# Kernel optimization log

Measured on AMD Instinct MI355X. Metric: run time of the kernel, lower is better.

Reference implementation:

```python
import jax, jax.numpy as jnp
import numpy as np

B, T, C = 4, 1024, 512
H, HD = 8, 64
NE, K = 8, 2
FF = 4 * C


def setup_inputs() -> dict:
    key = jax.random.key(0)
    ks = jax.random.split(key, 16)
    s = 0.02
    return {
        "x": jax.random.normal(ks[0], (B, T, C), jnp.float32),
        "ln1_g": jnp.ones((C,), jnp.float32),
        "ln1_b": jnp.zeros((C,), jnp.float32),
        "ln2_g": jnp.ones((C,), jnp.float32),
        "ln2_b": jnp.zeros((C,), jnp.float32),
        "Wq": jax.random.normal(ks[1], (H, C, HD), jnp.float32) * s,
        "Wk": jax.random.normal(ks[2], (H, C, HD), jnp.float32) * s,
        "Wv": jax.random.normal(ks[3], (H, C, HD), jnp.float32) * s,
        "Wp": jax.random.normal(ks[4], (H * HD, C), jnp.float32) * s,
        "bp": jnp.zeros((C,), jnp.float32),
        "Wr": jax.random.normal(ks[5], (C, NE), jnp.float32) * s,
        "br": jnp.zeros((NE,), jnp.float32),
        "W1": jax.random.normal(ks[6], (NE, C, FF), jnp.float32) * s,
        "b1": jnp.zeros((NE, FF), jnp.float32),
        "W2": jax.random.normal(ks[7], (NE, FF, C), jnp.float32) * s,
        "b2": jnp.zeros((NE, C), jnp.float32),
    }


def _ln(x, g, b, eps=1e-5):
    mu = jnp.mean(x, axis=-1, keepdims=True)
    var = jnp.var(x, axis=-1, keepdims=True)
    return (x - mu) * jax.lax.rsqrt(var + eps) * g + b


def reference(x, ln1_g, ln1_b, ln2_g, ln2_b, Wq, Wk, Wv, Wp, bp, Wr, br, W1, b1, W2, b2):
    # --- multi-head causal attention (all heads stacked) ---
    h = _ln(x, ln1_g, ln1_b)
    q = jnp.einsum("btc,hcd->bhtd", h, Wq)
    k = jnp.einsum("btc,hcd->bhtd", h, Wk)
    v = jnp.einsum("btc,hcd->bhtd", h, Wv)
    wei = jnp.einsum("bhtd,bhsd->bhts", q, k) / np.sqrt(HD).astype(np.float32)
    causal = jnp.tril(jnp.ones((T, T), bool))
    wei = jnp.where(causal, wei, -jnp.inf)
    wei = jax.nn.softmax(wei, axis=-1)
    attn = jnp.einsum("bhts,bhsd->bhtd", wei, v)  # [B,H,T,HD]
    attn = attn.transpose(0, 2, 1, 3).reshape(B, T, H * HD)
    x2 = x + attn @ Wp + bp

    # --- SparseMoE: dense all-experts compute, masked top-k combine ---
    h2 = _ln(x2, ln2_g, ln2_b)
    scores = h2 @ Wr + br  # [B,T,NE]
    topk_scores, indices = jax.lax.top_k(scores, K)
    # scatter top-k scores into zeros (rest stays 0), then softmax over experts
    mask = jnp.sum(jax.nn.one_hot(indices, NE, dtype=scores.dtype) * topk_scores[..., None], axis=-2)
    router = jax.nn.softmax(mask, axis=-1)  # [B,T,NE]
    hid = jax.nn.relu(jnp.einsum("btc,ecf->btef", h2, W1) + b1)  # [B,T,NE,FF]
    eo = jnp.einsum("btef,efc->btec", hid, W2) + b2  # [B,T,NE,C]
    moe = jnp.einsum("bte,btec->btc", router, eo)
    return x2 + moe
```

## Files before the change

kernel.cpp:

```cpp
#include <hip/hip_runtime.h>


typedef unsigned short u16;
typedef __attribute__((ext_vector_type(8))) short s16x8;
typedef __attribute__((ext_vector_type(4))) float f32x4;

__device__ __forceinline__ u16 f2bf(float f) {
  union { float f; unsigned u; } v; v.f = f;
  unsigned r = v.u + 0x7fffu + ((v.u >> 16) & 1u);
  return (u16)(r >> 16);
}
__device__ __forceinline__ float bf2f(u16 h) {
  union { unsigned u; float f; } v; v.u = ((unsigned)h) << 16;
  return v.f;
}

#define GLDS16(g, s) __builtin_amdgcn_global_load_lds( \
    (const __attribute__((address_space(1))) void*)(g), \
    (__attribute__((address_space(3))) void*)(s), 16, 0, 0)

#define MFMA16(a, b, c) __builtin_amdgcn_mfma_f32_16x16x32_bf16((a), (b), (c), 0, 0, 0)

__global__ __launch_bounds__(256) void transpose_k(
    const float* __restrict__ in, u16* __restrict__ out,
    int R, int C, long long ibs, long long obs, float scale)
{
  __shared__ float tile[32][33];
  in  += (long long)blockIdx.z * ibs;
  out += (long long)blockIdx.z * obs;
  const int c0 = blockIdx.x * 32, r0 = blockIdx.y * 32;
  const int tx = threadIdx.x, ty = threadIdx.y;
  #pragma unroll
  for (int i = 0; i < 4; ++i)
    tile[ty + i*8][tx] = in[(size_t)(r0 + ty + i*8) * C + c0 + tx];
  __syncthreads();
  #pragma unroll
  for (int i = 0; i < 4; ++i)
    out[(size_t)(c0 + ty + i*8) * R + r0 + tx] = f2bf(tile[tx][ty + i*8] * scale);
}

__global__ __launch_bounds__(256) void vtrans_k(
    const u16* __restrict__ qkv, u16* __restrict__ vt)
{
  __shared__ u16 tile[32][33];
  const int bh = blockIdx.z, b = bh >> 3, h = bh & 7;
  const int t0 = blockIdx.x * 32, d0 = blockIdx.y * 32;
  const int tx = threadIdx.x, ty = threadIdx.y;
  #pragma unroll
  for (int i = 0; i < 4; ++i)
    tile[ty + i*8][tx] = qkv[(size_t)(b*1024 + t0 + ty + i*8) * 1536 + 1024 + h*64 + d0 + tx];
  __syncthreads();
  #pragma unroll
  for (int i = 0; i < 4; ++i)
    vt[(size_t)bh*65536 + (size_t)(d0 + ty + i*8) * 1024 + t0 + tx] = tile[tx][ty + i*8];
}

__global__ __launch_bounds__(256) void ln_k(
    const float* __restrict__ x, const float* __restrict__ g,
    const float* __restrict__ b, u16* __restrict__ o)
{
  const int row = blockIdx.x, t = threadIdx.x;
  const float* xr = x + (size_t)row * 512;
  const float a0 = xr[t], a1 = xr[t + 256];
  float s = a0 + a1, ss = a0*a0 + a1*a1;
  #pragma unroll
  for (int off = 1; off < 64; off <<= 1) {
    s  += __shfl_xor(s, off);
    ss += __shfl_xor(ss, off);
  }
  __shared__ float rs[4], rq[4];
  const int w = t >> 6;
  if ((t & 63) == 0) { rs[w] = s; rq[w] = ss; }
  __syncthreads();
  s  = rs[0] + rs[1] + rs[2] + rs[3];
  ss = rq[0] + rq[1] + rq[2] + rq[3];
  const float mu = s * (1.f/512.f);
  const float var = ss * (1.f/512.f) - mu*mu;
  const float rstd = rsqrtf(var + 1e-5f);
  o[(size_t)row*512 + t]       = f2bf((a0 - mu) * rstd * g[t]     + b[t]);
  o[(size_t)row*512 + t + 256] = f2bf((a1 - mu) * rstd * g[t+256] + b[t+256]);
}

template<int EPI>
__global__ __launch_bounds__(256) void gemm64(
    const u16* __restrict__ A, const u16* __restrict__ Bt,
    int M, int N, int K, int lda, int ldb,
    u16* __restrict__ obf, float* __restrict__ oa,
    const float* __restrict__ bias, const float* __restrict__ extra, int e0)
{
  __shared__ u16 Asm[128*64];
  __shared__ u16 Bsm[128*64];
  const int t = threadIdx.x;
  const int l = t & 63;
  const int wid = t >> 6, wr = wid >> 1, wc = wid & 1;
  const int lrow = l & 15, lhi = l >> 4;
  const int m0 = blockIdx.x * 128, n0 = blockIdx.y * 128;

  const f32x4 z4 = {0.f, 0.f, 0.f, 0.f};
  f32x4 acc[4][4];
  #pragma unroll
  for (int i = 0; i < 4; ++i)
    #pragma unroll
    for (int j = 0; j < 4; ++j) acc[i][j] = z4;

  const u16* ga = A  + (size_t)(m0 + (t >> 3)) * lda + (t & 7) * 8;
  const u16* gb = Bt + (size_t)(n0 + (t >> 3)) * ldb + (t & 7) * 8;

  for (int k0 = 0; k0 < K; k0 += 64) {
    #pragma unroll
    for (int i = 0; i < 4; ++i) {
      GLDS16(ga + (size_t)i*32*lda + k0, (char*)Asm + i*4096 + t*16);
      GLDS16(gb + (size_t)i*32*ldb + k0, (char*)Bsm + i*4096 + t*16);
    }
    __syncthreads();
    #pragma unroll
    for (int kh = 0; kh < 2; ++kh) {
      s16x8 af[4], bfr[4];
      #pragma unroll
      for (int i = 0; i < 4; ++i)
        af[i]  = *(const s16x8*)(Asm + (wr*64 + i*16 + lrow)*64 + kh*32 + lhi*8);
      #pragma unroll
      for (int j = 0; j < 4; ++j)
        bfr[j] = *(const s16x8*)(Bsm + (wc*64 + j*16 + lrow)*64 + kh*32 + lhi*8);
      #pragma unroll
      for (int i = 0; i < 4; ++i)
        #pragma unroll
        for (int j = 0; j < 4; ++j)
          acc[i][j] = MFMA16(af[i], bfr[j], acc[i][j]);
    }
    __syncthreads();
  }

  #pragma unroll
  for (int i = 0; i < 4; ++i) {
    const int rbase = m0 + wr*64 + i*16 + lhi*4;
    #pragma unroll
    for (int j = 0; j < 4; ++j) {
      const int col = n0 + wc*64 + j*16 + lrow;
      #pragma unroll
      for (int rr = 0; rr < 4; ++rr) {
        const int row = rbase + rr;
        const float v = acc[i][j][rr];
        if (EPI == 0) {
          obf[(size_t)row*N + col] = f2bf(v);
        } else if (EPI == 1) {
          const float r = extra[(size_t)row*8 + e0 + (col >> 11)];
          obf[(size_t)row*N + col] = f2bf(fmaxf(v + bias[col], 0.f) * r);
        } else {
          oa[(size_t)row*N + col] = v + bias[col] + extra[(size_t)row*N + col];
        }
      }
    }
  }
}

template<int NKT, int EPI>
__global__ __launch_bounds__(512, 2) void gemm8p(
    const u16* __restrict__ A, const u16* __restrict__ Bt,
    int lda, int ldb,
    u16* __restrict__ obf,
    const float* __restrict__ bias, const float* __restrict__ rout)
{
  __shared__ u16 Lds[2][2][256*64];
  const int t = threadIdx.x, l = t & 63;
  const int wid = t >> 6, wm = wid >> 2, wn = wid & 3;
  const int lrow = l & 15, lhi = l >> 4;

  int m0, n0, zz = 0;
  {
    const int bid = blockIdx.x;
    const int r = bid & 7, k = bid >> 3;
    if (EPI == 1) { m0 = (k >> 3) * 256; n0 = (r * 8 + (k & 7)) * 256; }
    else { zz = r + (k >> 3) * 8; m0 = ((k & 7) >> 1) * 256; n0 = (k & 1) * 256; }
  }
  const u16* Ab = A  + (size_t)m0 * lda + (EPI == 4 ? zz * 512 : 0);
  const u16* Bb = Bt + (size_t)n0 * ldb + (EPI == 4 ? zz * 512 : 0);

  const int tr = t >> 3;
  const int sc = ((t & 7) ^ (tr & 7)) * 8;

#define STG(bf, kt, hx) do { \
    const int X_ = (hx) >> 1, h_ = (hx) & 1; \
    const u16* s_ = X_ ? Bb : Ab; \
    const int ld_ = X_ ? ldb : lda; \
    char* d_ = (char*)&Lds[bf][X_][0] + h_*16384 + t*16; \
    GLDS16(s_ + (size_t)(h_*128 + tr) * ld_ + (kt)*64 + sc, d_); \
    GLDS16(s_ + (size_t)(h_*128 + 64 + tr) * ld_ + (kt)*64 + sc, d_ + 8192); \
  } while (0)

#define RD(Ls, row, kb) (*(const s16x8*)((const char*)(Ls) + (row)*128 + ((kb) ^ (((row)&7)<<4))))

  f32x4 acc[8][4];
  const f32x4 z4 = {0.f, 0.f, 0.f, 0.f};
  #pragma unroll
  for (int i = 0; i < 8; ++i)
    #pragma unroll
    for (int j = 0; j < 4; ++j) acc[i][j] = z4;

  #pragma unroll
  for (int kt = 0; kt < 2; ++kt)
    #pragma unroll
    for (int hx = 0; hx < 4; ++hx) STG(kt & 1, kt, hx);
  asm volatile("s_waitcnt vmcnt(8)" ::: "memory");
  __builtin_amdgcn_sched_barrier(0);
  __builtin_amdgcn_s_barrier();

  s16x8 frA[2][4], frB[2][2];
  #pragma unroll
  for (int X = 0; X < NKT; ++X) {
    const u16* As = &Lds[X & 1][0][0];
    const u16* Bs = &Lds[X & 1][1][0];
    #pragma unroll
    for (int q = 0; q < 4; ++q) {
      const int mh = q >> 1, nh = q & 1;
      if (nh == 0) {
        #pragma unroll
        for (int kk = 0; kk < 2; ++kk)
          #pragma unroll
          for (int mf = 0; mf < 4; ++mf) {
            const int row = wm*128 + (mh*4 + mf)*16 + lrow;
            frA[kk][mf] = RD(As, row, kk*64 + lhi*16);
          }
      }
      #pragma unroll
      for (int kk = 0; kk < 2; ++kk)
        #pragma unroll
        for (int nf = 0; nf < 2; ++nf) {
          const int row = wn*64 + (nh*2 + nf)*16 + lrow;
          frB[kk][nf] = RD(Bs, row, kk*64 + lhi*16);
        }
      {
        const int P = 4*X + q;
        if (P >= 3) {
          const int kts = ((P - 3) >> 2) + 2, hh = (P - 3) & 3;
          if (kts < NKT) STG(kts & 1, kts, hh);
        }
      }
      __builtin_amdgcn_s_barrier();
      asm volatile("s_waitcnt lgkmcnt(0)" ::: "memory");
      __builtin_amdgcn_sched_barrier(0);
      __builtin_amdgcn_s_setprio(1);
      #pragma unroll
      for (int kk = 0; kk < 2; ++kk)
        #pragma unroll
        for (int mf = 0; mf < 4; ++mf)
          #pragma unroll
          for (int nf = 0; nf < 2; ++nf)
            acc[mh*4 + mf][nh*2 + nf] =
                MFMA16(frA[kk][mf], frB[kk][nf], acc[mh*4 + mf][nh*2 + nf]);
      __builtin_amdgcn_s_setprio(0);
      if (q == 3 && X + 1 < NKT) {
        if (X + 2 < NKT) asm volatile("s_waitcnt vmcnt(2)" ::: "memory");
        else             asm volatile("s_waitcnt vmcnt(0)" ::: "memory");
        __builtin_amdgcn_sched_barrier(0);
      }
      __builtin_amdgcn_s_barrier();
    }
  }
#undef STG
#undef RD

  u16* outp = (EPI == 4) ? obf + (size_t)zz * 1024 * 512 : obf;
  #pragma unroll
  for (int mf = 0; mf < 8; ++mf) {
    const int rbase = m0 + wm*128 + mf*16 + lhi*4;
    #pragma unroll
    for (int nf = 0; nf < 4; ++nf) {
      const int col = n0 + wn*64 + nf*16 + lrow;
      #pragma unroll
      for (int rr = 0; rr < 4; ++rr) {
        const int row = rbase + rr;
        const float v = acc[mf][nf][rr];
        if (EPI == 1) {
          const float r = rout[(size_t)row*8 + (col >> 11)];
          outp[(size_t)row*16384 + col] = f2bf(fmaxf(v + bias[col], 0.f) * r);
        } else {
          outp[(size_t)row*512 + col] = f2bf(v);
        }
      }
    }
  }
}

__global__ __launch_bounds__(256) void combineQ_k(
    float* __restrict__ outq, const u16* __restrict__ P,
    const float* __restrict__ routq, const float* __restrict__ b2)
{
  const int row = blockIdx.x, t = threadIdx.x;
  float r[8];
  #pragma unroll
  for (int e = 0; e < 8; ++e) r[e] = routq[(size_t)row*8 + e];
  #pragma unroll
  for (int cc = 0; cc < 2; ++cc) {
    const int c = t + cc*256;
    float v = outq[(size_t)row*512 + c];
    #pragma unroll
    for (int z = 0; z < 32; ++z) v += bf2f(P[(size_t)z*524288 + (size_t)row*512 + c]);
    #pragma unroll
    for (int e = 0; e < 8; ++e) v += r[e] * b2[(size_t)e*512 + c];
    outq[(size_t)row*512 + c] = v;
  }
}

__global__ __launch_bounds__(256) void gemm2_k(
    const u16* __restrict__ hid, const u16* __restrict__ w2t,
    u16* __restrict__ P, int e0, int accum)
{
  __shared__ u16 Asm[128*64];
  __shared__ u16 Bsm[64*64];
  const int t = threadIdx.x;
  const int l = t & 63;
  const int wid = t >> 6, wr = wid >> 1, wc = wid & 1;
  const int lrow = l & 15, lhi = l >> 4;
  const int m0 = blockIdx.x * 128, n0 = blockIdx.y * 64, z = blockIdx.z;

  const u16* A  = hid + z * 2048;
  const u16* Bt = w2t + (size_t)(e0 + z) * 512 * 2048;
  u16* Pz = P + (size_t)z * 4096 * 512;

  const f32x4 z4 = {0.f, 0.f, 0.f, 0.f};
  f32x4 acc[4][2];
  #pragma unroll
  for (int i = 0; i < 4; ++i) { acc[i][0] = z4; acc[i][1] = z4; }

  const u16* ga = A  + (size_t)(m0 + (t >> 3)) * 4096 + (t & 7) * 8;
  const u16* gb = Bt + (size_t)(n0 + (t >> 3)) * 2048 + (t & 7) * 8;

  for (int k0 = 0; k0 < 2048; k0 += 64) {
    #pragma unroll
    for (int i = 0; i < 4; ++i)
      GLDS16(ga + (size_t)i*32*4096 + k0, (char*)Asm + i*4096 + t*16);
    #pragma unroll
    for (int i = 0; i < 2; ++i)
      GLDS16(gb + (size_t)i*32*2048 + k0, (char*)Bsm + i*4096 + t*16);
    __syncthreads();
    #pragma unroll
    for (int kh = 0; kh < 2; ++kh) {
      s16x8 af[4], bfr[2];
      #pragma unroll
      for (int i = 0; i < 4; ++i)
        af[i]  = *(const s16x8*)(Asm + (wr*64 + i*16 + lrow)*64 + kh*32 + lhi*8);
      #pragma unroll
      for (int j = 0; j < 2; ++j)
        bfr[j] = *(const s16x8*)(Bsm + (wc*32 + j*16 + lrow)*64 + kh*32 + lhi*8);
      #pragma unroll
      for (int i = 0; i < 4; ++i)
        #pragma unroll
        for (int j = 0; j < 2; ++j)
          acc[i][j] = MFMA16(af[i], bfr[j], acc[i][j]);
    }
    __syncthreads();
  }

  #pragma unroll
  for (int i = 0; i < 4; ++i) {
    const int rbase = m0 + wr*64 + i*16 + lhi*4;
    #pragma unroll
    for (int j = 0; j < 2; ++j) {
      const int col = n0 + wc*32 + j*16 + lrow;
      #pragma unroll
      for (int rr = 0; rr < 4; ++rr) {
        const size_t idx = (size_t)(rbase + rr) * 512 + col;
        const float old = accum ? bf2f(Pz[idx]) : 0.f;
        Pz[idx] = f2bf(old + acc[i][j][rr]);
      }
    }
  }
}

__global__ __launch_bounds__(256) void combineB_k(
    float* __restrict__ out, const u16* __restrict__ P,
    const float* __restrict__ rout, const float* __restrict__ b2)
{
  const int row = blockIdx.x, t = threadIdx.x;
  float r[8];
  #pragma unroll
  for (int e = 0; e < 8; ++e) r[e] = rout[(size_t)row*8 + e];
  #pragma unroll
  for (int cc = 0; cc < 2; ++cc) {
    const int c = t + cc*256;
    const size_t idx = (size_t)row*512 + c;
    float v = out[idx] + bf2f(P[idx]) + bf2f(P[(size_t)4096*512 + idx]);
    #pragma unroll
    for (int e = 0; e < 8; ++e) v += r[e] * b2[(size_t)e*512 + c];
    out[idx] = v;
  }
}

__global__ __launch_bounds__(256) void attn_k(
    const u16* __restrict__ qkv, const u16* __restrict__ vt, u16* __restrict__ o)
{
  const int bid = blockIdx.x;
  const int xcd = bid & 7, rr_ = bid >> 3;
  const int bh = (rr_ >> 4) * 8 + xcd;
  const int qb = rr_ & 15;
  const int b = bh >> 3, h = bh & 7;
  const int t = threadIdx.x, l = t & 63, w = t >> 6;
  const int lrow = l & 15, lhi = l >> 4;
  const int t0w = qb*64 + w*16;

  __shared__ u16 Ksm[2][64*64];
  __shared__ u16 Vsm[2][64*64];
  __shared__ u16 Psm[4][16][72];

  const u16* qrow = qkv + (size_t)(b*1024 + t0w + lrow) * 1536 + h*64 + lhi*8;
  s16x8 qf0 = *(const s16x8*)qrow;
  s16x8 qf1 = *(const s16x8*)(qrow + 32);

  const f32x4 z4 = {0.f,0.f,0.f,0.f};
  float m[4], sl[4];
  f32x4 oacc[4];
  #pragma unroll
  for (int i = 0; i < 4; ++i) { m[i] = -1e30f; sl[i] = 0.f; oacc[i] = z4; }

  const int trow = t >> 3;
  const int csw = ((t & 7) ^ (trow & 7)) * 8;
  const u16* gk = qkv + (size_t)(b*1024 + trow) * 1536 + 512 + h*64 + csw;
  const u16* gv = vt + (size_t)bh*65536 + (size_t)trow*1024 + csw;
  const int nt = qb + 1;

#define ASTAGE(buf, s0) do { \
    _Pragma("unroll") \
    for (int i = 0; i < 2; ++i) { \
      GLDS16(gk + (size_t)((s0) + i*32) * 1536, (char*)Ksm[buf] + i*4096 + t*16); \
      GLDS16(gv + (s0) + (size_t)(i*32)*1024,   (char*)Vsm[buf] + i*4096 + t*16); \
    } } while (0)

  ASTAGE(0, 0);
  for (int kv = 0; kv < nt; ++kv) {
    const int s0 = kv * 64;
    if (kv + 1 < nt) {
      ASTAGE((kv + 1) & 1, s0 + 64);
      asm volatile("s_waitcnt vmcnt(4)" ::: "memory");
    } else {
      asm volatile("s_waitcnt vmcnt(0)" ::: "memory");
    }
    __builtin_amdgcn_s_barrier();
    __builtin_amdgcn_sched_barrier(0);
    const u16* Ks = Ksm[kv & 1];
    const u16* Vs = Vsm[kv & 1];

    f32x4 sacc[4] = {z4, z4, z4, z4};
    #pragma unroll
    for (int n = 0; n < 4; ++n) {
      const int r = n*16 + lrow;
      s16x8 kf0 = *(const s16x8*)((const char*)Ks + r*128 + ((lhi*16) ^ ((r & 7) << 4)));
      s16x8 kf1 = *(const s16x8*)((const char*)Ks + r*128 + ((64 + lhi*16) ^ ((r & 7) << 4)));
      sacc[n] = MFMA16(qf0, kf0, sacc[n]);
      sacc[n] = MFMA16(qf1, kf1, sacc[n]);
    }
    if (s0 + 63 > t0w) {
      #pragma unroll
      for (int n = 0; n < 4; ++n)
        #pragma unroll
        for (int rr = 0; rr < 4; ++rr)
          if (s0 + n*16 + lrow > t0w + lhi*4 + rr) sacc[n][rr] = -1e30f;
    }
    float pm[4];
    #pragma unroll
    for (int rr = 0; rr < 4; ++rr)
      pm[rr] = fmaxf(fmaxf(sacc[0][rr], sacc[1][rr]), fmaxf(sacc[2][rr], sacc[3][rr]));
    #pragma unroll
    for (int rr = 0; rr < 4; ++rr) {
      pm[rr] = fmaxf(pm[rr], __shfl_xor(pm[rr], 1));
      pm[rr] = fmaxf(pm[rr], __shfl_xor(pm[rr], 2));
      pm[rr] = fmaxf(pm[rr], __shfl_xor(pm[rr], 4));
      pm[rr] = fmaxf(pm[rr], __shfl_xor(pm[rr], 8));
    }
    float p[4][4], ps[4], scv[4];
    #pragma unroll
    for (int rr = 0; rr < 4; ++rr) {
      const float mn = fmaxf(m[rr], pm[rr]);
      scv[rr] = __expf(m[rr] - mn);
      m[rr] = mn;
      ps[rr] = 0.f;
      #pragma unroll
      for (int n = 0; n < 4; ++n) {
        p[n][rr] = __expf(sacc[n][rr] - mn);
        ps[rr] += p[n][rr];
      }
    }
    #pragma unroll
    for (int rr = 0; rr < 4; ++rr) {
      ps[rr] += __shfl_xor(ps[rr], 1);
      ps[rr] += __shfl_xor(ps[rr], 2);
      ps[rr] += __shfl_xor(ps[rr], 4);
      ps[rr] += __shfl_xor(ps[rr], 8);
      sl[rr] = sl[rr] * scv[rr] + ps[rr];
    }
    #pragma unroll
    for (int ct = 0; ct < 4; ++ct) {
      f32x4 t4 = oacc[ct];
      #pragma unroll
      for (int rr = 0; rr < 4; ++rr) t4[rr] *= scv[rr];
      oacc[ct] = t4;
    }
    #pragma unroll
    for (int n = 0; n < 4; ++n)
      #pragma unroll
      for (int rr = 0; rr < 4; ++rr)
        Psm[w][lhi*4 + rr][n*16 + lrow] = f2bf(p[n][rr]);
    asm volatile("s_waitcnt lgkmcnt(0)" ::: "memory");
    __builtin_amdgcn_sched_barrier(0);
    s16x8 pa0 = *(const s16x8*)&Psm[w][lrow][lhi*8];
    s16x8 pa1 = *(const s16x8*)&Psm[w][lrow][32 + lhi*8];
    #pragma unroll
    for (int ct = 0; ct < 4; ++ct) {
      const int r = ct*16 + lrow;
      s16x8 vb0 = *(const s16x8*)((const char*)Vs + r*128 + ((lhi*16) ^ ((r & 7) << 4)));
      s16x8 vb1 = *(const s16x8*)((const char*)Vs + r*128 + ((64 + lhi*16) ^ ((r & 7) << 4)));
      oacc[ct] = MFMA16(pa0, vb0, oacc[ct]);
      oacc[ct] = MFMA16(pa1, vb1, oacc[ct]);
    }
    __builtin_amdgcn_s_barrier();
    __builtin_amdgcn_sched_barrier(0);
  }
#undef ASTAGE
  #pragma unroll
  for (int ct = 0; ct < 4; ++ct)
    #pragma unroll
    for (int rr = 0; rr < 4; ++rr) {
      const int row = b*1024 + t0w + lhi*4 + rr;
      o[(size_t)row*512 + h*64 + ct*16 + lrow] = f2bf(oacc[ct][rr] / sl[rr]);
    }
}

__global__ __launch_bounds__(256) void router_k(
    const float* __restrict__ x2, const float* __restrict__ g,
    const float* __restrict__ b, const float* __restrict__ Wr,
    const float* __restrict__ br, float* __restrict__ rt)
{
  const int l = threadIdx.x & 63, w = threadIdx.x >> 6;
  const int tkn = blockIdx.x * 4 + w;
  const float* xr = x2 + (size_t)tkn * 512;
  float v[8];
  float s = 0.f, ss = 0.f;
  #pragma unroll
  for (int i = 0; i < 8; ++i) {
    v[i] = xr[l*8 + i];
    s += v[i]; ss += v[i]*v[i];
  }
  #pragma unroll
  for (int off = 1; off < 64; off <<= 1) {
    s  += __shfl_xor(s, off);
    ss += __shfl_xor(ss, off);
  }
  const float mu = s * (1.f/512.f);
  const float var = ss * (1.f/512.f) - mu*mu;
  const float rstd = rsqrtf(var + 1e-5f);
  float acc[8];
  #pragma unroll
  for (int e = 0; e < 8; ++e) acc[e] = 0.f;
  #pragma unroll
  for (int i = 0; i < 8; ++i) {
    const int c = l*8 + i;
    const float hv = (v[i] - mu) * rstd * g[c] + b[c];
    const float* wrow = Wr + (size_t)c * 8;
    #pragma unroll
    for (int e = 0; e < 8; ++e) acc[e] += hv * wrow[e];
  }
  #pragma unroll
  for (int e = 0; e < 8; ++e) {
    #pragma unroll
    for (int off = 1; off < 64; off <<= 1) acc[e] += __shfl_xor(acc[e], off);
    acc[e] += br[e];
  }
  int e1 = 0;
  #pragma unroll
  for (int e = 1; e < 8; ++e) if (acc[e] > acc[e1]) e1 = e;
  int e2 = (e1 == 0) ? 1 : 0;
  #pragma unroll
  for (int e = 0; e < 8; ++e) if (e != e1 && acc[e] > acc[e2]) e2 = e;
  const float mx = fmaxf(acc[e1], 0.f);
  float Z = 0.f;
  #pragma unroll
  for (int e = 0; e < 8; ++e) {
    const float mv = (e == e1 || e == e2) ? acc[e] : 0.f;
    Z += __expf(mv - mx);
  }
  if (l < 8) {
    const float mv = (l == e1 || l == e2) ? acc[l] : 0.f;
    rt[(size_t)tkn * 8 + l] = __expf(mv - mx) / Z;
  }
}

extern "C" void kernel_launch(void* const* d_in, const int* in_sizes, int n_in,
                              void* d_out, int out_size, void* d_ws, size_t ws_size,
                              hipStream_t stream) {
  const float* x    = (const float*)d_in[0];
  const float* ln1g = (const float*)d_in[1];
  const float* ln1b = (const float*)d_in[2];
  const float* ln2g = (const float*)d_in[3];
  const float* ln2b = (const float*)d_in[4];
  const float* Wq   = (const float*)d_in[5];
  const float* Wk   = (const float*)d_in[6];
  const float* Wv   = (const float*)d_in[7];
  const float* Wp   = (const float*)d_in[8];
  const float* bp   = (const float*)d_in[9];
  const float* Wr   = (const float*)d_in[10];
  const float* br   = (const float*)d_in[11];
  const float* W1   = (const float*)d_in[12];
  const float* b1   = (const float*)d_in[13];
  const float* W2   = (const float*)d_in[14];
  const float* b2   = (const float*)d_in[15];
  float* out = (float*)d_out;

  const int pathN = (ws_size >= (size_t)104988672) ? 1 : 0;

  char* ws = (char*)d_ws;
  size_t off = 0;
  auto alloc = [&](size_t bytes) -> char* {
    char* p = ws + off;
    off += (bytes + 255) & ~(size_t)255;
    return p;
  };
  u16* w1_t = (u16*)alloc((size_t)8*2048*512*2);
  u16* w2f  = (u16*)alloc((size_t)8*512*2048*2);
  u16* h2b  = (u16*)alloc((size_t)4096*512*2);
  float* rout = (float*)alloc((size_t)4096*8*4);
  u16* hidq = (u16*)alloc((size_t)4096*4096*2);
  u16* Ppl  = (u16*)alloc((size_t)2*4096*512*2);
  u16* wqkv_t = (u16*)hidq;
  u16* wp_t   = (u16*)((char*)hidq + 1572864);
  u16* hb     = (u16*)((char*)hidq + 2097152);
  u16* attnb  = (u16*)((char*)hidq + 6291456);
  u16* qkvb   = (u16*)((char*)hidq + 10485760);
  u16* vtb    = (u16*)((char*)hidq + 23068672);

  const dim3 tb(32, 8);
  transpose_k<<<dim3(2,16,8),  tb, 0, stream>>>(Wq, wqkv_t,              512,   64, 512*64,  (long long)64*512, 0.125f);
  transpose_k<<<dim3(2,16,8),  tb, 0, stream>>>(Wk, wqkv_t + 512*512,    512,   64, 512*64,  (long long)64*512, 1.f);
  transpose_k<<<dim3(2,16,8),  tb, 0, stream>>>(Wv, wqkv_t + 2*512*512,  512,   64, 512*64,  (long long)64*512, 1.f);
  transpose_k<<<dim3(16,16,1), tb, 0, stream>>>(Wp, wp_t,                512,  512, 0, 0, 1.f);
  transpose_k<<<dim3(64,16,8), tb, 0, stream>>>(W1, w1_t,                512, 2048, (long long)512*2048, (long long)2048*512, 1.f);
  if (pathN)
    transpose_k<<<dim3(16,512,1), tb, 0, stream>>>(W2, w2f, 16384, 512, 0, 0, 1.f);
  else
    transpose_k<<<dim3(16,64,8), tb, 0, stream>>>(W2, w2f, 2048, 512, (long long)2048*512, (long long)512*2048, 1.f);

  ln_k<<<4096, 256, 0, stream>>>(x, ln1g, ln1b, hb);
  gemm64<0><<<dim3(32,12), 256, 0, stream>>>(hb, wqkv_t, 4096, 1536, 512, 512, 512,
                                             qkvb, nullptr, nullptr, nullptr, 0);
  vtrans_k<<<dim3(32,2,32), tb, 0, stream>>>(qkvb, vtb);
  attn_k<<<512, 256, 0, stream>>>(qkvb, vtb, attnb);
  gemm64<2><<<dim3(32,4), 256, 0, stream>>>(attnb, wp_t, 4096, 512, 512, 512, 512,
                                            nullptr, out, bp, x, 0);
  ln_k<<<4096, 256, 0, stream>>>(out, ln2g, ln2b, h2b);
  router_k<<<1024, 256, 0, stream>>>(out, ln2g, ln2b, Wr, br, rout);

  if (pathN) {
    for (int q = 0; q < 4; ++q) {
      gemm8p<8,1><<<256, 512, 0, stream>>>(h2b + (size_t)q*1024*512, w1_t, 512, 512,
                                           hidq, b1, rout + (size_t)q*8192);
      gemm8p<8,4><<<256, 512, 0, stream>>>(hidq, w2f, 16384, 16384,
                                           Ppl, nullptr, nullptr);
      combineQ_k<<<1024, 256, 0, stream>>>(out + (size_t)q*1024*512, Ppl,
                                           rout + (size_t)q*8192, b2);
    }
  } else {
    for (int p = 0; p < 4; ++p) {
      const int e0 = 2*p;
      gemm64<1><<<dim3(32,32), 256, 0, stream>>>(h2b, w1_t + (size_t)e0*2048*512,
                                                 4096, 4096, 512, 512, 512,
                                                 hidq, nullptr, b1 + (size_t)e0*2048, rout, e0);
      gemm2_k<<<dim3(32,8,2), 256, 0, stream>>>(hidq, w2f, Ppl, e0, p > 0 ? 1 : 0);
    }
    combineB_k<<<4096, 256, 0, stream>>>(out, Ppl, rout, b2);
  }
}
```

Measured before the change: 327.5 us.

## Double-buffer GEMM loads, fuse QKV transposes and LN2 into router, vectorize combine

Replaces the single-buffered gemm64 with gemm2p, which double-buffers LDS tiles and waits on vmcnt so global loads of the next tile overlap MFMA work. The output projection now uses a 64-wide N tile, giving twice as many blocks. The three QKV weight transposes are merged into one launch, and the router kernel now also writes the bf16 LN2 output, which removes the separate ln_k pass. combineQ_k reads packed bf16 pairs, and Ppl is sized to 32 partials on pathN. The cost is doubled LDS per block, which may reduce occupancy.

Measured after the change: 314.7 us. -3.9%, faster.

```diff
diff --git a/kernel.cpp b/kernel.cpp
--- a/kernel.cpp
+++ b/kernel.cpp
@@ -37,6 +37,26 @@
   #pragma unroll
   for (int i = 0; i < 4; ++i)
     out[(size_t)(c0 + ty + i*8) * R + r0 + tx] = f2bf(tile[tx][ty + i*8] * scale);
+}
+
+__global__ __launch_bounds__(256) void transqkv_k(
+    const float* __restrict__ Wq, const float* __restrict__ Wk,
+    const float* __restrict__ Wv, u16* __restrict__ out)
+{
+  __shared__ float tile[32][33];
+  const int z = blockIdx.z, which = z >> 3, head = z & 7;
+  const float* in = (which == 0 ? Wq : (which == 1 ? Wk : Wv)) + (size_t)head * 512 * 64;
+  u16* o = out + (size_t)which * 512 * 512 + (size_t)head * 64 * 512;
+  const float scale = (which == 0) ? 0.125f : 1.f;
+  const int c0 = blockIdx.x * 32, r0 = blockIdx.y * 32;
+  const int tx = threadIdx.x, ty = threadIdx.y;
+  #pragma unroll
+  for (int i = 0; i < 4; ++i)
+    tile[ty + i*8][tx] = in[(size_t)(r0 + ty + i*8) * 64 + c0 + tx];
+  __syncthreads();
+  #pragma unroll
+  for (int i = 0; i < 4; ++i)
+    o[(size_t)(c0 + ty + i*8) * 512 + r0 + tx] = f2bf(tile[tx][ty + i*8] * scale);
 }
 
 __global__ __launch_bounds__(256) void vtrans_k(
@@ -81,62 +101,81 @@
   o[(size_t)row*512 + t + 256] = f2bf((a1 - mu) * rstd * g[t+256] + b[t+256]);
 }
 
-template<int EPI>
-__global__ __launch_bounds__(256) void gemm64(
+template<int BN, int EPI>
+__global__ __launch_bounds__(256) void gemm2p(
     const u16* __restrict__ A, const u16* __restrict__ Bt,
     int M, int N, int K, int lda, int ldb,
     u16* __restrict__ obf, float* __restrict__ oa,
     const float* __restrict__ bias, const float* __restrict__ extra, int e0)
 {
-  __shared__ u16 Asm[128*64];
-  __shared__ u16 Bsm[128*64];
-  const int t = threadIdx.x;
-  const int l = t & 63;
+  constexpr int NB = BN / 32;
+  constexpr int SB = BN / 32;
+  __shared__ u16 Asm[2][128*64];
+  __shared__ u16 Bsm[2][BN*64];
+  const int t = threadIdx.x, l = t & 63;
   const int wid = t >> 6, wr = wid >> 1, wc = wid & 1;
   const int lrow = l & 15, lhi = l >> 4;
-  const int m0 = blockIdx.x * 128, n0 = blockIdx.y * 128;
+  const int m0 = blockIdx.x * 128, n0 = blockIdx.y * BN;
 
   const f32x4 z4 = {0.f, 0.f, 0.f, 0.f};
-  f32x4 acc[4][4];
+  f32x4 acc[4][NB];
   #pragma unroll
   for (int i = 0; i < 4; ++i)
     #pragma unroll
-    for (int j = 0; j < 4; ++j) acc[i][j] = z4;
+    for (int j = 0; j < NB; ++j) acc[i][j] = z4;
 
   const u16* ga = A  + (size_t)(m0 + (t >> 3)) * lda + (t & 7) * 8;
   const u16* gb = Bt + (size_t)(n0 + (t >> 3)) * ldb + (t & 7) * 8;
 
-  for (int k0 = 0; k0 < K; k0 += 64) {
-    #pragma unroll
-    for (int i = 0; i < 4; ++i) {
-      GLDS16(ga + (size_t)i*32*lda + k0, (char*)Asm + i*4096 + t*16);
-      GLDS16(gb + (size_t)i*32*ldb + k0, (char*)Bsm + i*4096 + t*16);
-    }
-    __syncthreads();
+#define STG2(buf, k0) do { \
+    _Pragma("unroll") \
+    for (int i = 0; i < 4; ++i) \
+      GLDS16(ga + (size_t)(i*32)*lda + (k0), (char*)Asm[buf] + i*4096 + t*16); \
+    _Pragma("unroll") \
+    for (int i = 0; i < SB; ++i) \
+      GLDS16(gb + (size_t)(i*32)*ldb + (k0), (char*)Bsm[buf] + i*4096 + t*16); \
+  } while (0)
+
+  const int NT = K >> 6;
+  STG2(0, 0);
+  for (int tt = 0; tt < NT; ++tt) {
+    if (tt + 1 < NT) {
+      STG2((tt + 1) & 1, (tt + 1) * 64);
+      if constexpr (BN == 128) asm volatile("s_waitcnt vmcnt(8)" ::: "memory");
+      else                     asm volatile("s_waitcnt vmcnt(6)" ::: "memory");
+    } else {
+      asm volatile("s_waitcnt vmcnt(0)" ::: "memory");
+    }
+    __builtin_amdgcn_sched_barrier(0);
+    __builtin_amdgcn_s_barrier();
+    const u16* As = Asm[tt & 1];
+    const u16* Bs = Bsm[tt & 1];
     #pragma unroll
     for (int kh = 0; kh < 2; ++kh) {
-      s16x8 af[4], bfr[4];
+      s16x8 af[4], bfr[NB];
       #pragma unroll
       for (int i = 0; i < 4; ++i)
-        af[i]  = *(const s16x8*)(Asm + (wr*64 + i*16 + lrow)*64 + kh*32 + lhi*8);
-      #pragma unroll
-      for (int j = 0; j < 4; ++j)
-        bfr[j] = *(const s16x8*)(Bsm + (wc*64 + j*16 + lrow)*64 + kh*32 + lhi*8);
+        af[i]  = *(const s16x8*)(As + (wr*64 + i*16 + lrow)*64 + kh*32 + lhi*8);
+      #pragma unroll
+      for (int j = 0; j < NB; ++j)
+        bfr[j] = *(const s16x8*)(Bs + (wc*(BN/2) + j*16 + lrow)*64 + kh*32 + lhi*8);
       #pragma unroll
       for (int i = 0; i < 4; ++i)
         #pragma unroll
-        for (int j = 0; j < 4; ++j)
+        for (int j = 0; j < NB; ++j)
           acc[i][j] = MFMA16(af[i], bfr[j], acc[i][j]);
     }
-    __syncthreads();
-  }
+    __builtin_amdgcn_s_barrier();
+    __builtin_amdgcn_sched_barrier(0);
+  }
+#undef STG2
 
   #pragma unroll
   for (int i = 0; i < 4; ++i) {
     const int rbase = m0 + wr*64 + i*16 + lhi*4;
     #pragma unroll
-    for (int j = 0; j < 4; ++j) {
-      const int col = n0 + wc*64 + j*16 + lrow;
+    for (int j = 0; j < NB; ++j) {
+      const int col = n0 + wc*(BN/2) + j*16 + lrow;
       #pragma unroll
       for (int rr = 0; rr < 4; ++rr) {
         const int row = rbase + rr;
@@ -287,19 +326,25 @@
     const float* __restrict__ routq, const float* __restrict__ b2)
 {
   const int row = blockIdx.x, t = threadIdx.x;
+  const int c = t * 2;
   float r[8];
   #pragma unroll
   for (int e = 0; e < 8; ++e) r[e] = routq[(size_t)row*8 + e];
-  #pragma unroll
-  for (int cc = 0; cc < 2; ++cc) {
-    const int c = t + cc*256;
-    float v = outq[(size_t)row*512 + c];
-    #pragma unroll
-    for (int z = 0; z < 32; ++z) v += bf2f(P[(size_t)z*524288 + (size_t)row*512 + c]);
-    #pragma unroll
-    for (int e = 0; e < 8; ++e) v += r[e] * b2[(size_t)e*512 + c];
-    outq[(size_t)row*512 + c] = v;
-  }
+  float v0 = outq[(size_t)row*512 + c];
+  float v1 = outq[(size_t)row*512 + c + 1];
+  #pragma unroll
+  for (int z = 0; z < 32; ++z) {
+    const unsigned pv = *(const unsigned*)(P + (size_t)z*524288 + (size_t)row*512 + c);
+    v0 += bf2f((u16)(pv & 0xffffu));
+    v1 += bf2f((u16)(pv >> 16));
+  }
+  #pragma unroll
+  for (int e = 0; e < 8; ++e) {
+    v0 += r[e] * b2[(size_t)e*512 + c];
+    v1 += r[e] * b2[(size_t)e*512 + c + 1];
+  }
+  outq[(size_t)row*512 + c]     = v0;
+  outq[(size_t)row*512 + c + 1] = v1;
 }
 
 __global__ __launch_bounds__(256) void gemm2_k(
@@ -528,7 +573,8 @@
 __global__ __launch_bounds__(256) void router_k(
     const float* __restrict__ x2, const float* __restrict__ g,
     const float* __restrict__ b, const float* __restrict__ Wr,
-    const float* __restrict__ br, float* __restrict__ rt)
+    const float* __restrict__ br, float* __restrict__ rt,
+    u16* __restrict__ h2o)
 {
   const int l = threadIdx.x & 63, w = threadIdx.x >> 6;
   const int tkn = blockIdx.x * 4 + w;
@@ -551,14 +597,17 @@
   float acc[8];
   #pragma unroll
   for (int e = 0; e < 8; ++e) acc[e] = 0.f;
+  s16x8 hw;
   #pragma unroll
   for (int i = 0; i < 8; ++i) {
     const int c = l*8 + i;
     const float hv = (v[i] - mu) * rstd * g[c] + b[c];
+    hw[i] = (short)f2bf(hv);
     const float* wrow = Wr + (size_t)c * 8;
     #pragma unroll
     for (int e = 0; e < 8; ++e) acc[e] += hv * wrow[e];
   }
+  *(s16x8*)(h2o + (size_t)tkn*512 + l*8) = hw;
   #pragma unroll
   for (int e = 0; e < 8; ++e) {
     #pragma unroll
@@ -619,7 +668,8 @@
   u16* h2b  = (u16*)alloc((size_t)4096*512*2);
   float* rout = (float*)alloc((size_t)4096*8*4);
   u16* hidq = (u16*)alloc((size_t)4096*4096*2);
-  u16* Ppl  = (u16*)alloc((size_t)2*4096*512*2);
+  u16* Ppl  = (u16*)alloc(pathN ? (size_t)32*1024*512*2
+                                : (size_t)2*4096*512*2);
   u16* wqkv_t = (u16*)hidq;
   u16* wp_t   = (u16*)((char*)hidq + 1572864);
   u16* hb     = (u16*)((char*)hidq + 2097152);
@@ -628,25 +678,22 @@
   u16* vtb    = (u16*)((char*)hidq + 23068672);
 
   const dim3 tb(32, 8);
-  transpose_k<<<dim3(2,16,8),  tb, 0, stream>>>(Wq, wqkv_t,              512,   64, 512*64,  (long long)64*512, 0.125f);
-  transpose_k<<<dim3(2,16,8),  tb, 0, stream>>>(Wk, wqkv_t + 512*512,    512,   64, 512*64,  (long long)64*512, 1.f);
-  transpose_k<<<dim3(2,16,8),  tb, 0, stream>>>(Wv, wqkv_t + 2*512*512,  512,   64, 512*64,  (long long)64*512, 1.f);
-  transpose_k<<<dim3(16,16,1), tb, 0, stream>>>(Wp, wp_t,                512,  512, 0, 0, 1.f);
-  transpose_k<<<dim3(64,16,8), tb, 0, stream>>>(W1, w1_t,                512, 2048, (long long)512*2048, (long long)2048*512, 1.f);
+  transqkv_k<<<dim3(2,16,24), tb, 0, stream>>>(Wq, Wk, Wv, wqkv_t);
+  transpose_k<<<dim3(16,16,1), tb, 0, stream>>>(Wp, wp_t, 512, 512, 0, 0, 1.f);
+  transpose_k<<<dim3(64,16,8), tb, 0, stream>>>(W1, w1_t, 512, 2048, (long long)512*2048, (long long)2048*512, 1.f);
   if (pathN)
     transpose_k<<<dim3(16,512,1), tb, 0, stream>>>(W2, w2f, 16384, 512, 0, 0, 1.f);
   else
     transpose_k<<<dim3(16,64,8), tb, 0, stream>>>(W2, w2f, 2048, 512, (long long)2048*512, (long long)512*2048, 1.f);
 
   ln_k<<<4096, 256, 0, stream>>>(x, ln1g, ln1b, hb);
-  gemm64<0><<<dim3(32,12), 256, 0, stream>>>(hb, wqkv_t, 4096, 1536, 512, 512, 512,
-                                             qkvb, nullptr, nullptr, nullptr, 0);
+  gemm2p<128,0><<<dim3(32,12), 256, 0, stream>>>(hb, wqkv_t, 4096, 1536, 512, 512, 512,
+                                                 qkvb, nullptr, nullptr, nullptr, 0);
   vtrans_k<<<dim3(32,2,32), tb, 0, stream>>>(qkvb, vtb);
   attn_k<<<512, 256, 0, stream>>>(qkvb, vtb, attnb);
-  gemm64<2><<<dim3(32,4), 256, 0, stream>>>(attnb, wp_t, 4096, 512, 512, 512, 512,
-                                            nullptr, out, bp, x, 0);
-  ln_k<<<4096, 256, 0, stream>>>(out, ln2g, ln2b, h2b);
-  router_k<<<1024, 256, 0, stream>>>(out, ln2g, ln2b, Wr, br, rout);
+  gemm2p<64,2><<<dim3(32,8), 256, 0, stream>>>(attnb, wp_t, 4096, 512, 512, 512, 512,
+                                               nullptr, out, bp, x, 0);
+  router_k<<<1024, 256, 0, stream>>>(out, ln2g, ln2b, Wr, br, rout, h2b);
 
   if (pathN) {
     for (int q = 0; q < 4; ++q) {
@@ -660,9 +707,9 @@
   } else {
     for (int p = 0; p < 4; ++p) {
       const int e0 = 2*p;
-      gemm64<1><<<dim3(32,32), 256, 0, stream>>>(h2b, w1_t + (size_t)e0*2048*512,
-                                                 4096, 4096, 512, 512, 512,
-                                                 hidq, nullptr, b1 + (size_t)e0*2048, rout, e0);
+      gemm2p<128,1><<<dim3(32,32), 256, 0, stream>>>(h2b, w1_t + (size_t)e0*2048*512,
+                                                     4096, 4096, 512, 512, 512,
+                                                     hidq, nullptr, b1 + (size_t)e0*2048, rout, e0);
       gemm2_k<<<dim3(32,8,2), 256, 0, stream>>>(hidq, w2f, Ppl, e0, p > 0 ? 1 : 0);
     }
     combineB_k<<<4096, 256, 0, stream>>>(out, Ppl, rout, b2);
```
